# Performance work log

Measured on AMD Instinct MI355X. Metric: run time of the kernel, lower is better.

## Reference

```python
import jax, jax.numpy as jnp
import numpy as np

N = 10000   # nodes
E = 320000  # edges
D = 3000    # input genes
H1, H2 = 1024, 128
F1, F2, F3, F4 = 256, 512, 1024, 2048
BN_EPS = 1e-5

def setup_inputs() -> dict:
    key = jax.random.key(0)
    ks = jax.random.split(key, 30)
    rn = lambda k, s, sc=0.05: jax.random.normal(k, s, dtype=jnp.float32) * sc
    inp = {}
    inp["x"] = jax.random.normal(ks[0], (N, D), dtype=jnp.float32)
    inp["edge_w"] = jax.random.uniform(ks[1], (E,), dtype=jnp.float32)
    inp["W1"] = rn(ks[2], (D, H1))
    inp["W2"] = rn(ks[3], (H1, H2))
    inp["W3"] = rn(ks[4], (H1, H2))
    dims = [(H2, F1), (F1, F2), (F2, F3), (F3, F4), (F4, D)]
    for i, (di, do) in enumerate(dims, start=1):
        inp[f"fc{i}_w"] = rn(ks[4 + i], (di, do))
        inp[f"fc{i}_b"] = jnp.zeros((do,), jnp.float32)
        if i <= 4:
            inp[f"bn{i}_g"] = jnp.ones((do,), jnp.float32)
            inp[f"bn{i}_b"] = jnp.zeros((do,), jnp.float32)
    inp["edge_src"] = jax.random.randint(ks[20], (E,), 0, N)
    inp["edge_dst"] = jax.random.randint(ks[21], (E,), 0, N)
    return inp

def reference(x, edge_w, W1, W2, W3,
              fc1_w, fc1_b, bn1_g, bn1_b,
              fc2_w, fc2_b, bn2_g, bn2_b,
              fc3_w, fc3_b, bn3_g, bn3_b,
              fc4_w, fc4_b, bn4_g, bn4_b,
              fc5_w, fc5_b, edge_src, edge_dst):
    # sparse adjacency matmul: out[dst] += w * h[src]
    def spmm(h):
        return jax.ops.segment_sum(h[edge_src] * edge_w[:, None], edge_dst, num_segments=N)
    # GCN encoder: GraphConvolution = act(adj @ (x @ W)) (dropout inactive in eval)
    h1 = jax.nn.relu(spmm(x @ W1))
    mu = spmm(h1 @ W2)
    logvar = spmm(h1 @ W3)
    z = mu  # eval-mode reparameterize returns mu
    # inner-product adjacency decoder (act = identity)
    adj_rec = z @ z.T
    # FC stack: Linear -> BatchNorm(eval, running mean=0, var=1) -> ReLU
    inv = 1.0 / jnp.sqrt(jnp.float32(1.0 + BN_EPS))
    def fc(h, w, b, g, be):
        return jax.nn.relu((h @ w + b) * inv * g + be)
    o = fc(z, fc1_w, fc1_b, bn1_g, bn1_b)
    o = fc(o, fc2_w, fc2_b, bn2_g, bn2_b)
    o = fc(o, fc3_w, fc3_b, bn3_g, bn3_b)
    o = fc(o, fc4_w, fc4_b, bn4_g, bn4_b)
    x_rec = o @ fc5_w + fc5_b  # fc5: no batchnorm, identity act
    return (adj_rec, mu, logvar, z, x_rec)
```

## Files before the change

### kernel.cpp

```cpp
#include <hip/hip_runtime.h>
#include <stdint.h>

typedef unsigned short ushort_t;
typedef __attribute__((ext_vector_type(8))) short short8;
typedef __attribute__((ext_vector_type(4))) float f32x4;

#define N_NODES 10000
#define MP      10240
#define E_EDGES 320000
#define D_IN    3000
#define K1P     3008
#define H1      1024
#define H2      128

static __device__ __forceinline__ float b2f(ushort_t u) {
  union { uint32_t u; float f; } x; x.u = ((uint32_t)u) << 16; return x.f;
}
static __device__ __forceinline__ ushort_t f2b(float f) {
  union { float f; uint32_t u; } x; x.f = f;
  uint32_t r = x.u + 0x7FFF + ((x.u >> 16) & 1);
  return (ushort_t)(r >> 16);
}

static __device__ __forceinline__ void gload16(const void* g, void* l) {
  __builtin_amdgcn_global_load_lds(
      (const __attribute__((address_space(1))) uint32_t*)g,
      (__attribute__((address_space(3))) uint32_t*)l, 16, 0, 0);
}

__global__ void zero_k(int* p, int n) {
  int i = blockIdx.x * 256 + threadIdx.x;
  if (i < n) p[i] = 0;
}
__global__ void count_k(const int* __restrict__ ed, int* __restrict__ cnt) {
  int e = blockIdx.x * 256 + threadIdx.x;
  if (e < E_EDGES) atomicAdd(&cnt[ed[e]], 1);
}
__global__ void scan_k(const int* __restrict__ cnt, int* __restrict__ rs, int* __restrict__ cur) {
  __shared__ int sums[256];
  int t = threadIdx.x;
  const int per = 40;
  int base = t * per;
  int s = 0;
  for (int i = 0; i < per; i++) { int idx = base + i; if (idx < N_NODES) s += cnt[idx]; }
  sums[t] = s;
  __syncthreads();
  if (t == 0) { int run = 0; for (int i = 0; i < 256; i++) { int v = sums[i]; sums[i] = run; run += v; } }
  __syncthreads();
  int run = sums[t];
  for (int i = 0; i < per; i++) {
    int idx = base + i;
    if (idx < N_NODES) { rs[idx] = run; cur[idx] = run; run += cnt[idx]; }
  }
  if (t == 255) rs[N_NODES] = run;
}
__global__ void fill_k(const int* __restrict__ es, const int* __restrict__ ed,
                       const float* __restrict__ ew,
                       int* __restrict__ cur, int* __restrict__ psrc, float* __restrict__ pw) {
  int e = blockIdx.x * 256 + threadIdx.x;
  if (e >= E_EDGES) return;
  int d = ed[e];
  int pos = atomicAdd(&cur[d], 1);
  psrc[pos] = es[e];
  pw[pos] = ew[e];
}

__global__ void conv_x_k(const float* __restrict__ x, ushort_t* __restrict__ xb) {
  int g = blockIdx.x * 256 + threadIdx.x;
  int row = g / 376;
  int c8 = (g % 376) * 8;
  float v[8];
  if (row < N_NODES && c8 < 3000) {
    const float4 f0 = *(const float4*)(x + (size_t)row * 3000 + c8);
    const float4 f1 = *(const float4*)(x + (size_t)row * 3000 + c8 + 4);
    v[0]=f0.x; v[1]=f0.y; v[2]=f0.z; v[3]=f0.w;
    v[4]=f1.x; v[5]=f1.y; v[6]=f1.z; v[7]=f1.w;
  } else {
#pragma unroll
    for (int i = 0; i < 8; i++) v[i] = 0.f;
  }
  uint32_t o0 = (uint32_t)f2b(v[0]) | ((uint32_t)f2b(v[1]) << 16);
  uint32_t o1 = (uint32_t)f2b(v[2]) | ((uint32_t)f2b(v[3]) << 16);
  uint32_t o2 = (uint32_t)f2b(v[4]) | ((uint32_t)f2b(v[5]) << 16);
  uint32_t o3 = (uint32_t)f2b(v[6]) | ((uint32_t)f2b(v[7]) << 16);
  uint4 ov; ov.x=o0; ov.y=o1; ov.z=o2; ov.w=o3;
  *(uint4*)&xb[(size_t)row * K1P + c8] = ov;
}

struct Seg { const float* src; ushort_t* dst; int K, Nn, Kp, Np, tilesN, blk0; };
struct SegPack { Seg s[8]; };
__global__ void conv_w_all_k(SegPack P) {
  __shared__ float tile[32][33];
  int b = blockIdx.x;
  int si = 0;
#pragma unroll
  for (int i = 1; i < 8; ++i) if (b >= P.s[i].blk0) si = i;
  Seg sg = P.s[si];
  int rel = b - sg.blk0;
  int tk = rel / sg.tilesN, tn = rel % sg.tilesN;
  int tx = threadIdx.x & 31, ty0 = threadIdx.x >> 5;
#pragma unroll
  for (int i = 0; i < 4; ++i) {
    int ty = ty0 + i * 8;
    int k = tk * 32 + ty, n = tn * 32 + tx;
    tile[ty][tx] = (k < sg.K && n < sg.Nn) ? sg.src[(size_t)k * sg.Nn + n] : 0.f;
  }
  __syncthreads();
#pragma unroll
  for (int i = 0; i < 4; ++i) {
    int ty = ty0 + i * 8;
    int n = tn * 32 + ty, k = tk * 32 + tx;
    sg.dst[(size_t)n * sg.Kp + k] = f2b(tile[tx][ty]);
  }
}

template<int EPI>
__global__ __launch_bounds__(256)
void gemm_bt(const ushort_t* __restrict__ A, const ushort_t* __restrict__ BT, int K,
             void* __restrict__ outp, int ldOut, int realM, int realN,
             const float* __restrict__ bias, const float* __restrict__ bng,
             const float* __restrict__ bnb)
{
  __shared__ ushort_t lA[128 * 32];
  __shared__ ushort_t lB[128 * 32];
  const int tid  = threadIdx.x;
  const int row0 = blockIdx.x * 128;
  const int col0 = blockIdx.y * 128;
  const int lane = tid & 63;
  const int wave = tid >> 6;
  const int wr = (wave >> 1) * 64, wc = (wave & 1) * 64;
  const int fr = lane & 15, fq = lane >> 4;

  f32x4 acc[4][4] = {};

  const int rA = tid >> 2;
  const int cA = (tid & 3) * 8;
  const ushort_t* Ab = A  + (size_t)(row0 + rA) * K + cA;
  const ushort_t* Bb = BT + (size_t)(col0 + rA) * K + cA;
  ushort_t* lA0 = &lA[tid * 8];
  ushort_t* lA1 = &lA[2048 + tid * 8];
  ushort_t* lB0 = &lB[tid * 8];
  ushort_t* lB1 = &lB[2048 + tid * 8];
  const size_t rstep = (size_t)64 * K;

  for (int k0 = 0; k0 < K; k0 += 32) {
    gload16(Ab + k0,         lA0);
    gload16(Ab + rstep + k0, lA1);
    gload16(Bb + k0,         lB0);
    gload16(Bb + rstep + k0, lB1);
    __syncthreads();
    short8 af[4], bv[4];
#pragma unroll
    for (int m = 0; m < 4; m++) af[m] = *(const short8*)&lA[(wr + m * 16 + fr) * 32 + fq * 8];
#pragma unroll
    for (int n = 0; n < 4; n++) bv[n] = *(const short8*)&lB[(wc + n * 16 + fr) * 32 + fq * 8];
#pragma unroll
    for (int m = 0; m < 4; m++)
#pragma unroll
      for (int n = 0; n < 4; n++)
        acc[m][n] = __builtin_amdgcn_mfma_f32_16x16x32_bf16(af[m], bv[n], acc[m][n], 0, 0, 0);
    __syncthreads();
  }

  const float inv = 0.9999950000374997f;
#pragma unroll
  for (int n = 0; n < 4; n++) {
    int col = col0 + wc + n * 16 + fr;
    float s = 0.f, t = 0.f, bb = 0.f;
    if (EPI == 1) { s = inv * bng[col]; t = bias[col] * s + bnb[col]; }
    if (EPI == 2) { bb = (col < realN) ? bias[col] : 0.f; }
#pragma unroll
    for (int m = 0; m < 4; m++) {
      int rowb = row0 + wr + m * 16 + fq * 4;
#pragma unroll
      for (int r = 0; r < 4; r++) {
        int row = rowb + r;
        float v = acc[m][n][r];
        if (EPI == 0) {
          ((ushort_t*)outp)[(size_t)row * ldOut + col] = f2b(v);
        } else if (EPI == 1) {
          v = fmaxf(v * s + t, 0.f);
          ((ushort_t*)outp)[(size_t)row * ldOut + col] = f2b(v);
        } else if (EPI == 2) {
          if (row < realM && col < realN)
            ((float*)outp)[(size_t)row * ldOut + col] = v + bb;
        } else {
          if (row < realM && col < realN)
            ((float*)outp)[(size_t)row * ldOut + col] = v;
        }
      }
    }
  }
}

template<int EPI, int REP = 1>
__global__ __launch_bounds__(256, 2)
void gemm3(const ushort_t* __restrict__ A, const ushort_t* __restrict__ BT, int K,
           void* __restrict__ outp, int ldOut, int realM, int realN,
           const float* __restrict__ bias, const float* __restrict__ bng,
           const float* __restrict__ bnb)
{
  __shared__ ushort_t lA[3 * 128 * 32];
  __shared__ ushort_t lB[3 * 256 * 32];
  const int tid = threadIdx.x;
  const int wn  = tid >> 6;
  const int fr  = tid & 15, fq = (tid >> 4) & 3;

  int gx = gridDim.x;
  int nwg = gx * gridDim.y;
  int bid = blockIdx.y * gx + blockIdx.x;
  int q8 = nwg >> 3, r8 = nwg & 7;
  int xcd = bid & 7, j = bid >> 3;
  int swz = (xcd < r8 ? xcd * (q8 + 1) : r8 * (q8 + 1) + (xcd - r8) * q8) + j;
  const int row0 = (swz % gx) * 128;
  const int col0 = (swz / gx) * 256;

  auto stA = [&](int p, int kt, int r) {
    int c = r * 256 + tid;
    int row = c >> 2, slot = c & 3;
    int ss = slot ^ ((row >> 1) & 3);
    gload16(A + (size_t)(row0 + row) * K + kt * 32 + ss * 8,
            &lA[p * (128 * 32) + c * 8]);
  };
  auto stB = [&](int p, int kt, int r) {
    int c = r * 256 + tid;
    int row = c >> 2, slot = c & 3;
    int ss = slot ^ ((row >> 1) & 3);
    gload16(BT + (size_t)(col0 + row) * K + kt * 32 + ss * 8,
            &lB[p * (256 * 32) + c * 8]);
  };
  auto stage = [&](int p, int kt) {
    stA(p, kt, 0); stA(p, kt, 1);
    stB(p, kt, 0); stB(p, kt, 1); stB(p, kt, 2); stB(p, kt, 3);
  };

  const int NT = K >> 5;

  for (int rep = 0; rep < REP; ++rep) {
    if (REP > 1) {
      asm volatile("s_waitcnt vmcnt(0)" ::: "memory");
      __builtin_amdgcn_s_barrier();
      asm volatile("" ::: "memory");
    }
    f32x4 acc[8][4] = {};

    stage(0, 0);
    stage(1, 1);

    for (int t = 0; t < NT; ++t) {
      const int p = t % 3;
      const int s = (t + 2) % 3;
      const int ts = (t + 2 < NT) ? t + 2 : NT - 1;
      asm volatile("s_waitcnt vmcnt(6)" ::: "memory");
      __builtin_amdgcn_s_barrier();
      asm volatile("" ::: "memory");
      stage(s, ts);

      short8 bf[4], af[8];
#pragma unroll
      for (int n = 0; n < 4; ++n) {
        int rb = wn * 64 + n * 16 + fr;
        bf[n] = *(const short8*)&lB[p * (256 * 32) + rb * 32 + ((fq ^ ((rb >> 1) & 3)) * 8)];
      }
#pragma unroll
      for (int m = 0; m < 8; ++m) {
        int ra = m * 16 + fr;
        af[m] = *(const short8*)&lA[p * (128 * 32) + ra * 32 + ((fq ^ ((ra >> 1) & 3)) * 8)];
      }
      __builtin_amdgcn_s_setprio(1);
#pragma unroll
      for (int m = 0; m < 8; ++m)
#pragma unroll
        for (int n = 0; n < 4; ++n)
          acc[m][n] = __builtin_amdgcn_mfma_f32_16x16x32_bf16(af[m], bf[n], acc[m][n], 0, 0, 0);
      __builtin_amdgcn_s_setprio(0);
      asm volatile("" ::: "memory");
    }

    const float inv = 0.9999950000374997f;
#pragma unroll
    for (int n = 0; n < 4; ++n) {
      int col = col0 + wn * 64 + n * 16 + fr;
      float sc = 0.f, tc = 0.f, bb = 0.f;
      if (EPI == 1) { sc = inv * bng[col]; tc = bias[col] * sc + bnb[col]; }
      if (EPI == 2) { bb = (col < realN) ? bias[col] : 0.f; }
#pragma unroll
      for (int m = 0; m < 8; ++m) {
        int rowb = row0 + m * 16 + fq * 4;
        if (EPI == 4) {
          if (col < realN && rowb < realM) {
            if (rowb + 4 <= realM) {
              float4 v4; v4.x = acc[m][n][0]; v4.y = acc[m][n][1];
              v4.z = acc[m][n][2]; v4.w = acc[m][n][3];
              *(float4*)((float*)outp + (size_t)col * ldOut + rowb) = v4;
            } else {
              for (int r = 0; r < realM - rowb; ++r)
                ((float*)outp)[(size_t)col * ldOut + rowb + r] = acc[m][n][r];
            }
          }
        } else {
#pragma unroll
          for (int r = 0; r < 4; ++r) {
            int row = rowb + r;
            float v = acc[m][n][r];
            if (EPI == 0) {
              ((ushort_t*)outp)[(size_t)row * ldOut + col] = f2b(v);
            } else if (EPI == 1) {
              v = fmaxf(v * sc + tc, 0.f);
              ((ushort_t*)outp)[(size_t)row * ldOut + col] = f2b(v);
            } else if (EPI == 2) {
              if (row < realM && col < realN)
                ((float*)outp)[(size_t)row * ldOut + col] = v + bb;
            }
          }
        }
      }
    }
    asm volatile("" ::: "memory");
  }
}

__global__ void spmm1c_k(const ushort_t* __restrict__ h, ushort_t* __restrict__ o,
                         const int* __restrict__ rs, const int* __restrict__ psrc,
                         const float* __restrict__ pw) {
  const int chunk = blockIdx.y;
  const int dst = blockIdx.x * 4 + (threadIdx.x >> 6);
  const int lane = threadIdx.x & 63;
  const int c0 = chunk * 128 + lane * 2;
  float a0 = 0.f, a1 = 0.f;
  if (dst < N_NODES) {
    const int s0 = rs[dst], e0 = rs[dst + 1];
    int i = s0;
    for (; i + 8 <= e0; i += 8) {
      int   sr[8]; float wv[8]; uint32_t v[8];
#pragma unroll
      for (int u = 0; u < 8; ++u) { sr[u] = psrc[i + u]; wv[u] = pw[i + u]; }
#pragma unroll
      for (int u = 0; u < 8; ++u) v[u] = *(const uint32_t*)&h[(size_t)sr[u] * H1 + c0];
#pragma unroll
      for (int u = 0; u < 8; ++u) {
        a0 += wv[u] * b2f((ushort_t)(v[u] & 0xffff));
        a1 += wv[u] * b2f((ushort_t)(v[u] >> 16));
      }
    }
    for (; i < e0; ++i) {
      float wv = pw[i];
      uint32_t v = *(const uint32_t*)&h[(size_t)psrc[i] * H1 + c0];
      a0 += wv * b2f((ushort_t)(v & 0xffff));
      a1 += wv * b2f((ushort_t)(v >> 16));
    }
  }
  uint32_t ov = (uint32_t)f2b(fmaxf(a0, 0.f)) | ((uint32_t)f2b(fmaxf(a1, 0.f)) << 16);
  *(uint32_t*)&o[(size_t)dst * H1 + c0] = ov;
}

__global__ void spmm2_k(const ushort_t* __restrict__ pre, float* __restrict__ mu,
                        float* __restrict__ lv, float* __restrict__ zf,
                        ushort_t* __restrict__ zb,
                        const int* __restrict__ rs, const int* __restrict__ psrc,
                        const float* __restrict__ pw) {
  const int dst = blockIdx.x * 4 + (threadIdx.x >> 6);
  const int lane = threadIdx.x & 63;
  const int c0 = lane * 4;
  float a0 = 0.f, a1 = 0.f, a2 = 0.f, a3 = 0.f;
  if (dst < N_NODES) {
    const int s0 = rs[dst], e0 = rs[dst + 1];
    int i = s0;
    for (; i + 8 <= e0; i += 8) {
      int sr[8]; float wv[8]; uint2 v[8];
#pragma unroll
      for (int u = 0; u < 8; ++u) { sr[u] = psrc[i + u]; wv[u] = pw[i + u]; }
#pragma unroll
      for (int u = 0; u < 8; ++u) v[u] = *(const uint2*)&pre[(size_t)sr[u] * 256 + c0];
#pragma unroll
      for (int u = 0; u < 8; ++u) {
        a0 += wv[u] * b2f((ushort_t)(v[u].x & 0xffff));
        a1 += wv[u] * b2f((ushort_t)(v[u].x >> 16));
        a2 += wv[u] * b2f((ushort_t)(v[u].y & 0xffff));
        a3 += wv[u] * b2f((ushort_t)(v[u].y >> 16));
      }
    }
    for (; i < e0; ++i) {
      float wv = pw[i];
      uint2 v = *(const uint2*)&pre[(size_t)psrc[i] * 256 + c0];
      a0 += wv * b2f((ushort_t)(v.x & 0xffff));
      a1 += wv * b2f((ushort_t)(v.x >> 16));
      a2 += wv * b2f((ushort_t)(v.y & 0xffff));
      a3 += wv * b2f((ushort_t)(v.y >> 16));
    }
  }
  if (lane < 32) {
    uint2 zv;
    zv.x = (uint32_t)f2b(a0) | ((uint32_t)f2b(a1) << 16);
    zv.y = (uint32_t)f2b(a2) | ((uint32_t)f2b(a3) << 16);
    *(uint2*)&zb[(size_t)dst * 128 + c0] = zv;
    if (dst < N_NODES) {
      float4 m4; m4.x = a0; m4.y = a1; m4.z = a2; m4.w = a3;
      *(float4*)&mu[(size_t)dst * 128 + c0] = m4;
      *(float4*)&zf[(size_t)dst * 128 + c0] = m4;
    }
  } else if (dst < N_NODES) {
    float4 l4; l4.x = a0; l4.y = a1; l4.z = a2; l4.w = a3;
    *(float4*)&lv[(size_t)dst * 128 + (c0 - 128)] = l4;
  }
}

extern "C" void kernel_launch(void* const* d_in, const int* in_sizes, int n_in,
                              void* d_out, int out_size, void* d_ws, size_t ws_size,
                              hipStream_t stream) {
  (void)in_sizes; (void)n_in; (void)out_size; (void)ws_size;
  const float* x  = (const float*)d_in[0];
  const float* ew = (const float*)d_in[1];
  const float* W1 = (const float*)d_in[2];
  const float* W2 = (const float*)d_in[3];
  const float* W3 = (const float*)d_in[4];
  const float* fc_w[5] = {(const float*)d_in[5], (const float*)d_in[9],  (const float*)d_in[13], (const float*)d_in[17], (const float*)d_in[21]};
  const float* fc_b[5] = {(const float*)d_in[6], (const float*)d_in[10], (const float*)d_in[14], (const float*)d_in[18], (const float*)d_in[22]};
  const float* bn_g[4] = {(const float*)d_in[7], (const float*)d_in[11], (const float*)d_in[15], (const float*)d_in[19]};
  const float* bn_b[4] = {(const float*)d_in[8], (const float*)d_in[12], (const float*)d_in[16], (const float*)d_in[20]};
  const int* esrc = (const int*)d_in[23];
  const int* edst = (const int*)d_in[24];
  float* out = (float*)d_out;

  float* out_adj = out;
  float* out_mu  = out + (size_t)100000000;
  float* out_lv  = out + (size_t)101280000;
  float* out_z   = out + (size_t)102560000;
  float* out_xr  = out + (size_t)103840000;

  char* w = (char*)d_ws;
  size_t off = 0;
  auto alloc = [&](size_t bytes) { size_t o = off; off = (off + bytes + 255) & ~(size_t)255; return o; };
  int*      cnt  = (int*)(w + alloc(4 * N_NODES));
  int*      rs   = (int*)(w + alloc(4 * (N_NODES + 1)));
  int*      cur  = (int*)(w + alloc(4 * N_NODES));
  int*      psrc = (int*)(w + alloc(4 * E_EDGES));
  float*    pw   = (float*)(w + alloc(4 * E_EDGES));
  ushort_t* w1T  = (ushort_t*)(w + alloc((size_t)2 * 1024 * K1P));
  ushort_t* w23T = (ushort_t*)(w + alloc((size_t)2 * 256 * 1024));
  ushort_t* f1T  = (ushort_t*)(w + alloc((size_t)2 * 256 * 128));
  ushort_t* f2T  = (ushort_t*)(w + alloc((size_t)2 * 512 * 256));
  ushort_t* f3T  = (ushort_t*)(w + alloc((size_t)2 * 1024 * 512));
  ushort_t* f4T  = (ushort_t*)(w + alloc((size_t)2 * 2048 * 1024));
  ushort_t* f5T  = (ushort_t*)(w + alloc((size_t)2 * 3072 * 2048));
  ushort_t* xb   = (ushort_t*)(w + alloc((size_t)2 * MP * K1P));
  ushort_t* xw1b = (ushort_t*)(w + alloc((size_t)2 * MP * H1));
  ushort_t* h1b  = (ushort_t*)(w + alloc((size_t)2 * MP * H1));
  ushort_t* preb = (ushort_t*)(w + alloc((size_t)2 * MP * 256));
  ushort_t* zb   = (ushort_t*)(w + alloc((size_t)2 * MP * 128));
  ushort_t* act1 = xw1b;
  ushort_t* act2 = xb;
  ushort_t* act3 = h1b;
  ushort_t* act4 = xb;

  zero_k<<<(N_NODES + 255) / 256, 256, 0, stream>>>(cnt, N_NODES);
  count_k<<<(E_EDGES + 255) / 256, 256, 0, stream>>>(edst, cnt);
  scan_k<<<1, 256, 0, stream>>>(cnt, rs, cur);
  fill_k<<<(E_EDGES + 255) / 256, 256, 0, stream>>>(esrc, edst, ew, cur, psrc, pw);

  conv_x_k<<<(MP * 376) / 256, 256, 0, stream>>>(x, xb);
  {
    SegPack P;
    int b0 = 0;
    auto mk = [&](const float* s, ushort_t* d, int K, int Nn, int Kp, int Np) {
      Seg sg; sg.src = s; sg.dst = d; sg.K = K; sg.Nn = Nn; sg.Kp = Kp; sg.Np = Np;
      sg.tilesN = Np / 32; sg.blk0 = b0;
      b0 += (Kp / 32) * (Np / 32);
      return sg;
    };
    P.s[0] = mk(W1,      w1T,                       D_IN, 1024, K1P,  1024);
    P.s[1] = mk(W2,      w23T,                      1024, 128,  1024, 128);
    P.s[2] = mk(W3,      w23T + (size_t)128 * 1024, 1024, 128,  1024, 128);
    P.s[3] = mk(fc_w[0], f1T,                       128,  256,  128,  256);
    P.s[4] = mk(fc_w[1], f2T,                       256,  512,  256,  512);
    P.s[5] = mk(fc_w[2], f3T,                       512,  1024, 512,  1024);
    P.s[6] = mk(fc_w[3], f4T,                       1024, 2048, 1024, 2048);
    P.s[7] = mk(fc_w[4], f5T,                       2048, 3000, 2048, 3072);
    conv_w_all_k<<<b0, 256, 0, stream>>>(P);
  }

  dim3 blk2(256);
  gemm3<0><<<dim3(MP / 128, 1024 / 256), blk2, 0, stream>>>(xb, w1T, K1P, xw1b, 1024, MP, 1024, nullptr, nullptr, nullptr);
  spmm1c_k<<<dim3(MP / 4, 8), blk2, 0, stream>>>(xw1b, h1b, rs, psrc, pw);
  gemm_bt<0><<<dim3(MP / 128, 2), blk2, 0, stream>>>(h1b, w23T, 1024, preb, 256, MP, 256, nullptr, nullptr, nullptr);
  spmm2_k<<<dim3(MP / 4), blk2, 0, stream>>>(preb, out_mu, out_lv, out_z, zb, rs, psrc, pw);
  gemm3<4><<<dim3(MP / 128, MP / 256), blk2, 0, stream>>>(zb, zb, 128, out_adj, 10000, N_NODES, N_NODES, nullptr, nullptr, nullptr);
  gemm_bt<1><<<dim3(MP / 128, 2), blk2, 0, stream>>>(zb,   f1T, 128,  act1, 256,  MP, 256,  fc_b[0], bn_g[0], bn_b[0]);
  gemm_bt<1><<<dim3(MP / 128, 4), blk2, 0, stream>>>(act1, f2T, 256,  act2, 512,  MP, 512,  fc_b[1], bn_g[1], bn_b[1]);
  gemm3<1><<<dim3(MP / 128, 1024 / 256), blk2, 0, stream>>>(act2, f3T, 512,  act3, 1024, MP, 1024, fc_b[2], bn_g[2], bn_b[2]);
  gemm3<1><<<dim3(MP / 128, 2048 / 256), blk2, 0, stream>>>(act3, f4T, 1024, act4, 2048, MP, 2048, fc_b[3], bn_g[3], bn_b[3]);
  gemm3<2><<<dim3(MP / 128, 3072 / 256), blk2, 0, stream>>>(act4, f5T, 2048, out_xr, 3000, N_NODES, 3000, fc_b[4], nullptr, nullptr);
}
```

Before: 800.2 us.

## Add triple-buffered 256x128 GEMM kernel with XCD swizzle for large GEMMs

Adds a new gemm4 kernel that uses 512 threads, a 256x128 output tile, a three-stage LDS ring buffer with interleaved global prefetch, and wave priority hints around the MFMA bursts. It also remaps block IDs so neighbouring tiles land on the same XCD. The new kernel replaces gemm3 for the X@W1 GEMM and the fc3, fc4 and fc5 layers. The aim is to hide global-load latency behind MFMA work and to improve L2 reuse. In exchange it uses much more LDS (about 144 KB) with one block per CU, which may lower occupancy and leave fewer blocks available to fill the GPU.

```diff
diff --git a/kernel.cpp b/kernel.cpp
--- a/kernel.cpp
+++ b/kernel.cpp
@@ -317,6 +317,144 @@
       }
     }
     asm volatile("" ::: "memory");
+  }
+}
+
+#define G4_TA (256 * 64)
+#define G4_TB (128 * 64)
+template<int EPI>
+__global__ __launch_bounds__(512, 1)
+void gemm4(const ushort_t* __restrict__ A, const ushort_t* __restrict__ BT, int K,
+           void* __restrict__ outp, int ldOut, int realM, int realN,
+           const float* __restrict__ bias, const float* __restrict__ bng,
+           const float* __restrict__ bnb)
+{
+  __shared__ ushort_t lA[3 * G4_TA];
+  __shared__ ushort_t lB[3 * G4_TB];
+  const int tid = threadIdx.x;
+  const int wid = tid >> 6;
+  const int wm  = wid >> 1;
+  const int wn  = wid & 1;
+  const int fr  = tid & 15, fq = (tid >> 4) & 3;
+
+  int gx = gridDim.x;
+  int nwg = gx * gridDim.y;
+  int bid = blockIdx.y * gx + blockIdx.x;
+  int q8 = nwg >> 3, r8 = nwg & 7;
+  int xcd = bid & 7, j = bid >> 3;
+  int swz = (xcd < r8 ? xcd * (q8 + 1) : r8 * (q8 + 1) + (xcd - r8) * q8) + j;
+  const int row0 = (swz % gx) * 256;
+  const int col0 = (swz / gx) * 128;
+
+  auto stA = [&](int p, int kt, int r) {
+    int c = r * 512 + tid;
+    int cs = c & 63;
+    int cl = cs ^ (((cs >> 5) & 1) << 1);
+    int s  = c >> 6;
+    int row = (s >> 1) * 16 + (cl >> 2);
+    int kc  = (s & 1) * 4 + (cl & 3);
+    gload16(A + (size_t)(row0 + row) * K + kt * 64 + kc * 8,
+            &lA[p * G4_TA + c * 8]);
+  };
+  auto stB = [&](int p, int kt, int r) {
+    int c = r * 512 + tid;
+    int cs = c & 63;
+    int cl = cs ^ (((cs >> 5) & 1) << 1);
+    int s  = c >> 6;
+    int row = (s >> 1) * 16 + (cl >> 2);
+    int kc  = (s & 1) * 4 + (cl & 3);
+    gload16(BT + (size_t)(col0 + row) * K + kt * 64 + kc * 8,
+            &lB[p * G4_TB + c * 8]);
+  };
+
+  const int le = (fr * 32 + fq * 8) ^ (((fr >> 3) & 1) << 4);
+
+  f32x4 acc[4][4] = {};
+
+  const int NT = K >> 6;
+  stA(0,0,0); stA(0,0,1); stA(0,0,2); stA(0,0,3); stB(0,0,0); stB(0,0,1);
+  stA(1,1,0); stA(1,1,1); stA(1,1,2); stA(1,1,3); stB(1,1,0); stB(1,1,1);
+
+  for (int t = 0; t < NT; ++t) {
+    const int p = t % 3;
+    const int s = (t + 2) % 3;
+    const int ts = (t + 2 < NT) ? t + 2 : NT - 1;
+    asm volatile("s_waitcnt vmcnt(6)" ::: "memory");
+    __builtin_amdgcn_s_barrier();
+    asm volatile("" ::: "memory");
+
+    const ushort_t* pa = &lA[p * G4_TA];
+    const ushort_t* pb = &lB[p * G4_TB];
+
+    short8 a_[4][2];
+    {
+      short8 b_[2];
+#pragma unroll
+      for (int m = 0; m < 4; ++m)
+#pragma unroll
+        for (int kk = 0; kk < 2; ++kk)
+          a_[m][kk] = *(const short8*)&pa[((wm * 4 + m) * 2 + kk) * 512 + le];
+#pragma unroll
+      for (int kk = 0; kk < 2; ++kk)
+        b_[kk] = *(const short8*)&pb[((wn * 4 + 0) * 2 + kk) * 512 + le];
+      stA(s, ts, 0); stA(s, ts, 1);
+      asm volatile("s_waitcnt lgkmcnt(0)" ::: "memory");
+      __builtin_amdgcn_sched_barrier(0);
+      __builtin_amdgcn_s_setprio(1);
+#pragma unroll
+      for (int m = 0; m < 4; ++m)
+#pragma unroll
+        for (int kk = 0; kk < 2; ++kk)
+          acc[m][0] = __builtin_amdgcn_mfma_f32_16x16x32_bf16(a_[m][kk], b_[kk], acc[m][0], 0, 0, 0);
+      __builtin_amdgcn_s_setprio(0);
+    }
+#pragma unroll
+    for (int n = 1; n < 4; ++n) {
+      short8 b_[2];
+#pragma unroll
+      for (int kk = 0; kk < 2; ++kk)
+        b_[kk] = *(const short8*)&pb[((wn * 4 + n) * 2 + kk) * 512 + le];
+      if (n == 1)      { stA(s, ts, 2); stA(s, ts, 3); }
+      else if (n == 2) { stB(s, ts, 0); }
+      else             { stB(s, ts, 1); }
+      asm volatile("s_waitcnt lgkmcnt(0)" ::: "memory");
+      __builtin_amdgcn_sched_barrier(0);
+      __builtin_amdgcn_s_setprio(1);
+#pragma unroll
+      for (int m = 0; m < 4; ++m)
+#pragma unroll
+        for (int kk = 0; kk < 2; ++kk)
+          acc[m][n] = __builtin_amdgcn_mfma_f32_16x16x32_bf16(a_[m][kk], b_[kk], acc[m][n], 0, 0, 0);
+      __builtin_amdgcn_s_setprio(0);
+    }
+    asm volatile("" ::: "memory");
+  }
+
+  const float inv = 0.9999950000374997f;
+#pragma unroll
+  for (int n = 0; n < 4; ++n) {
+    int col = col0 + wn * 64 + n * 16 + fr;
+    float sc = 0.f, tc = 0.f, bb = 0.f;
+    if (EPI == 1) { sc = inv * bng[col]; tc = bias[col] * sc + bnb[col]; }
+    if (EPI == 2) { bb = (col < realN) ? bias[col] : 0.f; }
+#pragma unroll
+    for (int m = 0; m < 4; ++m) {
+      int rowb = row0 + wm * 64 + m * 16 + fq * 4;
+#pragma unroll
+      for (int r = 0; r < 4; ++r) {
+        int row = rowb + r;
+        float v = acc[m][n][r];
+        if (EPI == 0) {
+          ((ushort_t*)outp)[(size_t)row * ldOut + col] = f2b(v);
+        } else if (EPI == 1) {
+          v = fmaxf(v * sc + tc, 0.f);
+          ((ushort_t*)outp)[(size_t)row * ldOut + col] = f2b(v);
+        } else if (EPI == 2) {
+          if (row < realM && col < realN)
+            ((float*)outp)[(size_t)row * ldOut + col] = v + bb;
+        }
+      }
+    }
   }
 }
 
@@ -479,15 +617,15 @@
     conv_w_all_k<<<b0, 256, 0, stream>>>(P);
   }
 
-  dim3 blk2(256);
-  gemm3<0><<<dim3(MP / 128, 1024 / 256), blk2, 0, stream>>>(xb, w1T, K1P, xw1b, 1024, MP, 1024, nullptr, nullptr, nullptr);
+  dim3 blk2(256), blk5(512);
+  gemm4<0><<<dim3(MP / 256, 1024 / 128), blk5, 0, stream>>>(xb, w1T, K1P, xw1b, 1024, MP, 1024, nullptr, nullptr, nullptr);
   spmm1c_k<<<dim3(MP / 4, 8), blk2, 0, stream>>>(xw1b, h1b, rs, psrc, pw);
   gemm_bt<0><<<dim3(MP / 128, 2), blk2, 0, stream>>>(h1b, w23T, 1024, preb, 256, MP, 256, nullptr, nullptr, nullptr);
   spmm2_k<<<dim3(MP / 4), blk2, 0, stream>>>(preb, out_mu, out_lv, out_z, zb, rs, psrc, pw);
   gemm3<4><<<dim3(MP / 128, MP / 256), blk2, 0, stream>>>(zb, zb, 128, out_adj, 10000, N_NODES, N_NODES, nullptr, nullptr, nullptr);
   gemm_bt<1><<<dim3(MP / 128, 2), blk2, 0, stream>>>(zb,   f1T, 128,  act1, 256,  MP, 256,  fc_b[0], bn_g[0], bn_b[0]);
   gemm_bt<1><<<dim3(MP / 128, 4), blk2, 0, stream>>>(act1, f2T, 256,  act2, 512,  MP, 512,  fc_b[1], bn_g[1], bn_b[1]);
-  gemm3<1><<<dim3(MP / 128, 1024 / 256), blk2, 0, stream>>>(act2, f3T, 512,  act3, 1024, MP, 1024, fc_b[2], bn_g[2], bn_b[2]);
-  gemm3<1><<<dim3(MP / 128, 2048 / 256), blk2, 0, stream>>>(act3, f4T, 1024, act4, 2048, MP, 2048, fc_b[3], bn_g[3], bn_b[3]);
-  gemm3<2><<<dim3(MP / 128, 3072 / 256), blk2, 0, stream>>>(act4, f5T, 2048, out_xr, 3000, N_NODES, 3000, fc_b[4], nullptr, nullptr);
-}
+  gemm4<1><<<dim3(MP / 256, 1024 / 128), blk5, 0, stream>>>(act2, f3T, 512,  act3, 1024, MP, 1024, fc_b[2], bn_g[2], bn_b[2]);
+  gemm4<1><<<dim3(MP / 256, 2048 / 128), blk5, 0, stream>>>(act3, f4T, 1024, act4, 2048, MP, 2048, fc_b[3], bn_g[3], bn_b[3]);
+  gemm4<2><<<dim3(MP / 256, 3072 / 128), blk5, 0, stream>>>(act4, f5T, 2048, out_xr, 3000, N_NODES, 3000, fc_b[4], nullptr, nullptr);
+}
```

Result: slower. 840.9 us (+5.1%).

## Interleave adjacency-reconstruction tiles into fc4 and fc5 GEMM launches

Applied to the files above, without the earlier changes.

Removes the standalone z·zT GEMM launch and spreads its 3200 output tiles across the fc4 and fc5 GEMM grids. Blocks are assigned either an FC tile or an adjacency tile by proportional interleaving. The short-K, store-heavy adjacency work can then overlap with the compute-heavy long-K FC tiles. The cost is losing the XCD-aware swizzle for the FC tiles in the mixed kernels, plus more complex block scheduling.

```diff
diff --git a/kernel.cpp b/kernel.cpp
--- a/kernel.cpp
+++ b/kernel.cpp
@@ -193,27 +193,19 @@
   }
 }
 
-template<int EPI, int REP = 1>
-__global__ __launch_bounds__(256, 2)
-void gemm3(const ushort_t* __restrict__ A, const ushort_t* __restrict__ BT, int K,
-           void* __restrict__ outp, int ldOut, int realM, int realN,
-           const float* __restrict__ bias, const float* __restrict__ bng,
-           const float* __restrict__ bnb)
+template<int EPI>
+static __device__ __forceinline__
+void gemm3_body(const ushort_t* __restrict__ A, const ushort_t* __restrict__ BT, int K,
+                void* __restrict__ outp, int ldOut, int realM, int realN,
+                const float* __restrict__ bias, const float* __restrict__ bng,
+                const float* __restrict__ bnb, int row0, int col0,
+                ushort_t* lA, ushort_t* lB)
 {
-  __shared__ ushort_t lA[3 * 128 * 32];
-  __shared__ ushort_t lB[3 * 256 * 32];
   const int tid = threadIdx.x;
   const int wn  = tid >> 6;
   const int fr  = tid & 15, fq = (tid >> 4) & 3;
 
-  int gx = gridDim.x;
-  int nwg = gx * gridDim.y;
-  int bid = blockIdx.y * gx + blockIdx.x;
-  int q8 = nwg >> 3, r8 = nwg & 7;
-  int xcd = bid & 7, j = bid >> 3;
-  int swz = (xcd < r8 ? xcd * (q8 + 1) : r8 * (q8 + 1) + (xcd - r8) * q8) + j;
-  const int row0 = (swz % gx) * 128;
-  const int col0 = (swz / gx) * 256;
+  f32x4 acc[8][4] = {};
 
   auto stA = [&](int p, int kt, int r) {
     int c = r * 256 + tid;
@@ -235,88 +227,124 @@
   };
 
   const int NT = K >> 5;
-
-  for (int rep = 0; rep < REP; ++rep) {
-    if (REP > 1) {
-      asm volatile("s_waitcnt vmcnt(0)" ::: "memory");
-      __builtin_amdgcn_s_barrier();
-      asm volatile("" ::: "memory");
-    }
-    f32x4 acc[8][4] = {};
-
-    stage(0, 0);
-    stage(1, 1);
-
-    for (int t = 0; t < NT; ++t) {
-      const int p = t % 3;
-      const int s = (t + 2) % 3;
-      const int ts = (t + 2 < NT) ? t + 2 : NT - 1;
-      asm volatile("s_waitcnt vmcnt(6)" ::: "memory");
-      __builtin_amdgcn_s_barrier();
-      asm volatile("" ::: "memory");
-      stage(s, ts);
-
-      short8 bf[4], af[8];
-#pragma unroll
-      for (int n = 0; n < 4; ++n) {
-        int rb = wn * 64 + n * 16 + fr;
-        bf[n] = *(const short8*)&lB[p * (256 * 32) + rb * 32 + ((fq ^ ((rb >> 1) & 3)) * 8)];
-      }
-#pragma unroll
-      for (int m = 0; m < 8; ++m) {
-        int ra = m * 16 + fr;
-        af[m] = *(const short8*)&lA[p * (128 * 32) + ra * 32 + ((fq ^ ((ra >> 1) & 3)) * 8)];
-      }
-      __builtin_amdgcn_s_setprio(1);
-#pragma unroll
-      for (int m = 0; m < 8; ++m)
-#pragma unroll
-        for (int n = 0; n < 4; ++n)
-          acc[m][n] = __builtin_amdgcn_mfma_f32_16x16x32_bf16(af[m], bf[n], acc[m][n], 0, 0, 0);
-      __builtin_amdgcn_s_setprio(0);
-      asm volatile("" ::: "memory");
-    }
-
-    const float inv = 0.9999950000374997f;
+  stage(0, 0);
+  stage(1, 1);
+
+  for (int t = 0; t < NT; ++t) {
+    const int p = t % 3;
+    const int s = (t + 2) % 3;
+    const int ts = (t + 2 < NT) ? t + 2 : NT - 1;
+    asm volatile("s_waitcnt vmcnt(6)" ::: "memory");
+    __builtin_amdgcn_s_barrier();
+    asm volatile("" ::: "memory");
+    stage(s, ts);
+
+    short8 bf[4], af[8];
 #pragma unroll
     for (int n = 0; n < 4; ++n) {
-      int col = col0 + wn * 64 + n * 16 + fr;
-      float sc = 0.f, tc = 0.f, bb = 0.f;
-      if (EPI == 1) { sc = inv * bng[col]; tc = bias[col] * sc + bnb[col]; }
-      if (EPI == 2) { bb = (col < realN) ? bias[col] : 0.f; }
-#pragma unroll
-      for (int m = 0; m < 8; ++m) {
-        int rowb = row0 + m * 16 + fq * 4;
-        if (EPI == 4) {
-          if (col < realN && rowb < realM) {
-            if (rowb + 4 <= realM) {
-              float4 v4; v4.x = acc[m][n][0]; v4.y = acc[m][n][1];
-              v4.z = acc[m][n][2]; v4.w = acc[m][n][3];
-              *(float4*)((float*)outp + (size_t)col * ldOut + rowb) = v4;
-            } else {
-              for (int r = 0; r < realM - rowb; ++r)
-                ((float*)outp)[(size_t)col * ldOut + rowb + r] = acc[m][n][r];
-            }
+      int rb = wn * 64 + n * 16 + fr;
+      bf[n] = *(const short8*)&lB[p * (256 * 32) + rb * 32 + ((fq ^ ((rb >> 1) & 3)) * 8)];
+    }
+#pragma unroll
+    for (int m = 0; m < 8; ++m) {
+      int ra = m * 16 + fr;
+      af[m] = *(const short8*)&lA[p * (128 * 32) + ra * 32 + ((fq ^ ((ra >> 1) & 3)) * 8)];
+    }
+    __builtin_amdgcn_s_setprio(1);
+#pragma unroll
+    for (int m = 0; m < 8; ++m)
+#pragma unroll
+      for (int n = 0; n < 4; ++n)
+        acc[m][n] = __builtin_amdgcn_mfma_f32_16x16x32_bf16(af[m], bf[n], acc[m][n], 0, 0, 0);
+    __builtin_amdgcn_s_setprio(0);
+    asm volatile("" ::: "memory");
+  }
+
+  const float inv = 0.9999950000374997f;
+#pragma unroll
+  for (int n = 0; n < 4; ++n) {
+    int col = col0 + wn * 64 + n * 16 + fr;
+    float sc = 0.f, tc = 0.f, bb = 0.f;
+    if (EPI == 1) { sc = inv * bng[col]; tc = bias[col] * sc + bnb[col]; }
+    if (EPI == 2) { bb = (col < realN) ? bias[col] : 0.f; }
+#pragma unroll
+    for (int m = 0; m < 8; ++m) {
+      int rowb = row0 + m * 16 + fq * 4;
+      if (EPI == 4) {
+        if (col < realN && rowb < realM) {
+          if (rowb + 4 <= realM) {
+            float4 v4; v4.x = acc[m][n][0]; v4.y = acc[m][n][1];
+            v4.z = acc[m][n][2]; v4.w = acc[m][n][3];
+            *(float4*)((float*)outp + (size_t)col * ldOut + rowb) = v4;
+          } else {
+            for (int r = 0; r < realM - rowb; ++r)
+              ((float*)outp)[(size_t)col * ldOut + rowb + r] = acc[m][n][r];
           }
-        } else {
-#pragma unroll
-          for (int r = 0; r < 4; ++r) {
-            int row = rowb + r;
-            float v = acc[m][n][r];
-            if (EPI == 0) {
-              ((ushort_t*)outp)[(size_t)row * ldOut + col] = f2b(v);
-            } else if (EPI == 1) {
-              v = fmaxf(v * sc + tc, 0.f);
-              ((ushort_t*)outp)[(size_t)row * ldOut + col] = f2b(v);
-            } else if (EPI == 2) {
-              if (row < realM && col < realN)
-                ((float*)outp)[(size_t)row * ldOut + col] = v + bb;
-            }
+        }
+      } else {
+#pragma unroll
+        for (int r = 0; r < 4; ++r) {
+          int row = rowb + r;
+          float v = acc[m][n][r];
+          if (EPI == 0) {
+            ((ushort_t*)outp)[(size_t)row * ldOut + col] = f2b(v);
+          } else if (EPI == 1) {
+            v = fmaxf(v * sc + tc, 0.f);
+            ((ushort_t*)outp)[(size_t)row * ldOut + col] = f2b(v);
+          } else if (EPI == 2) {
+            if (row < realM && col < realN)
+              ((float*)outp)[(size_t)row * ldOut + col] = v + bb;
           }
         }
       }
     }
-    asm volatile("" ::: "memory");
+  }
+}
+
+template<int EPI>
+__global__ __launch_bounds__(256, 2)
+void gemm3(const ushort_t* __restrict__ A, const ushort_t* __restrict__ BT, int K,
+           void* __restrict__ outp, int ldOut, int realM, int realN,
+           const float* __restrict__ bias, const float* __restrict__ bng,
+           const float* __restrict__ bnb)
+{
+  __shared__ ushort_t lA[3 * 128 * 32];
+  __shared__ ushort_t lB[3 * 256 * 32];
+  int gx = gridDim.x;
+  int nwg = gx * gridDim.y;
+  int bid = blockIdx.y * gx + blockIdx.x;
+  int q8 = nwg >> 3, r8 = nwg & 7;
+  int xcd = bid & 7, j = bid >> 3;
+  int swz = (xcd < r8 ? xcd * (q8 + 1) : r8 * (q8 + 1) + (xcd - r8) * q8) + j;
+  const int row0 = (swz % gx) * 128;
+  const int col0 = (swz / gx) * 256;
+  gemm3_body<EPI>(A, BT, K, outp, ldOut, realM, realN, bias, bng, bnb, row0, col0, lA, lB);
+}
+
+template<int EPIFC>
+__global__ __launch_bounds__(256, 2)
+void gemm3_mix(const ushort_t* __restrict__ A, const ushort_t* __restrict__ BT, int K,
+               void* __restrict__ outp, int ldOut, int realM, int realN,
+               const float* __restrict__ bias, const float* __restrict__ bng,
+               const float* __restrict__ bnb,
+               const ushort_t* __restrict__ zbp, float* __restrict__ out_adj,
+               int nFC, int adjBase)
+{
+  __shared__ ushort_t lA[3 * 128 * 32];
+  __shared__ ushort_t lB[3 * 256 * 32];
+  const int T = gridDim.x * gridDim.y;
+  const int o = blockIdx.y * gridDim.x + blockIdx.x;
+  const int F0 = (o * nFC) / T;
+  const int F1 = ((o + 1) * nFC) / T;
+  if (F1 > F0) {
+    int row0 = (F0 % 80) * 128;
+    int col0 = (F0 / 80) * 256;
+    gemm3_body<EPIFC>(A, BT, K, outp, ldOut, realM, realN, bias, bng, bnb, row0, col0, lA, lB);
+  } else {
+    int a = adjBase + (o - F0);
+    if (a >= 3200) return;
+    gemm3_body<4>(zbp, zbp, 128, out_adj, 10000, 10000, 10000,
+                  nullptr, nullptr, nullptr, (a % 80) * 128, (a / 80) * 256, lA, lB);
   }
 }
 
@@ -484,10 +512,12 @@
   spmm1c_k<<<dim3(MP / 4, 8), blk2, 0, stream>>>(xw1b, h1b, rs, psrc, pw);
   gemm_bt<0><<<dim3(MP / 128, 2), blk2, 0, stream>>>(h1b, w23T, 1024, preb, 256, MP, 256, nullptr, nullptr, nullptr);
   spmm2_k<<<dim3(MP / 4), blk2, 0, stream>>>(preb, out_mu, out_lv, out_z, zb, rs, psrc, pw);
-  gemm3<4><<<dim3(MP / 128, MP / 256), blk2, 0, stream>>>(zb, zb, 128, out_adj, 10000, N_NODES, N_NODES, nullptr, nullptr, nullptr);
+
   gemm_bt<1><<<dim3(MP / 128, 2), blk2, 0, stream>>>(zb,   f1T, 128,  act1, 256,  MP, 256,  fc_b[0], bn_g[0], bn_b[0]);
   gemm_bt<1><<<dim3(MP / 128, 4), blk2, 0, stream>>>(act1, f2T, 256,  act2, 512,  MP, 512,  fc_b[1], bn_g[1], bn_b[1]);
   gemm3<1><<<dim3(MP / 128, 1024 / 256), blk2, 0, stream>>>(act2, f3T, 512,  act3, 1024, MP, 1024, fc_b[2], bn_g[2], bn_b[2]);
-  gemm3<1><<<dim3(MP / 128, 2048 / 256), blk2, 0, stream>>>(act3, f4T, 1024, act4, 2048, MP, 2048, fc_b[3], bn_g[3], bn_b[3]);
-  gemm3<2><<<dim3(MP / 128, 3072 / 256), blk2, 0, stream>>>(act4, f5T, 2048, out_xr, 3000, N_NODES, 3000, fc_b[4], nullptr, nullptr);
-}
+  gemm3_mix<1><<<dim3(80, 26), blk2, 0, stream>>>(act3, f4T, 1024, act4, 2048, MP, 2048,
+      fc_b[3], bn_g[3], bn_b[3], zb, out_adj, 640, 0);
+  gemm3_mix<2><<<dim3(80, 34), blk2, 0, stream>>>(act4, f5T, 2048, out_xr, 3000, N_NODES, 3000,
+      fc_b[4], nullptr, nullptr, zb, out_adj, 960, 1440);
+}
```

Result: slower. 816.5 us (+2.0%).
